# Optimization experiments

Measured on AMD Instinct MI355X. Metric: run time of the kernel, lower is better.

The kernel has to match this reference:

```python
import jax, jax.numpy as jnp
import numpy as np

LN_EPS = 1e-5

def setup_inputs() -> dict:
    key = jax.random.key(0)
    ks = jax.random.split(key, 4)
    B, D, H, K = 8192, 4096, 2048, 512
    return {
        "x": jax.random.normal(ks[0], (B, D), jnp.float32),
        "beta": jax.random.normal(ks[1], (D, K), jnp.float32) * 0.01,
        "compound_mean": jnp.zeros((D,), jnp.float32),
        "W1": jax.random.normal(ks[2], (H, D), jnp.float32) * 0.02,
        "b1": jnp.zeros((H,), jnp.float32),
        "ln_w": jnp.ones((H,), jnp.float32),
        "ln_b": jnp.zeros((H,), jnp.float32),
        "W2": jax.random.normal(ks[3], (K, H), jnp.float32) * 0.02,
        "b2": jnp.zeros((K,), jnp.float32),
    }

def reference(x, beta, compound_mean, W1, b1, ln_w, ln_b, W2, b2):
    # compound path of BiQBMVAE.forward (compound=True)
    h = jnp.einsum('bd,hd->bh', x - compound_mean, W1) + b1      # fc1
    mu = jnp.mean(h, axis=-1, keepdims=True)                      # LayerNorm
    var = jnp.mean(jnp.square(h - mu), axis=-1, keepdims=True)
    h = (h - mu) * jax.lax.rsqrt(var + LN_EPS) * ln_w + ln_b
    h = jax.nn.relu(h)                                            # act_fn
    q_logits = jnp.einsum('bh,kh->bk', h, W2) + b2                # fc2 -> [B, k]
    x_recon = jax.nn.sigmoid(jnp.einsum('bk,dk->bd', q_logits, beta))  # decode_compound
    return (q_logits, x_recon, q_logits, q_logits)
```

## Files before the change

kernel.cpp:

```cpp
#include <hip/hip_runtime.h>
#include <hip/hip_bf16.h>
#include <cstddef>
#include <cstdint>

#define LN_EPS 1e-5f

#define B_DIM 8192
#define D_DIM 4096
#define H_DIM 2048
#define K_DIM 512

typedef __bf16 bf16x8_t __attribute__((ext_vector_type(8)));
typedef float f32x4_t __attribute__((ext_vector_type(4)));

__device__ __forceinline__ void gl2lds16(const __hip_bfloat16* g,
                                         __hip_bfloat16* l) {
  __builtin_amdgcn_global_load_lds(
      (const __attribute__((address_space(1))) uint32_t*)g,
      (__attribute__((address_space(3))) uint32_t*)l, 16, 0, 0);
}

__global__ __launch_bounds__(256) void conv_x_kernel(
    const float* __restrict__ x, const float* __restrict__ cmean,
    __hip_bfloat16* __restrict__ out) {
  const long i = (((long)blockIdx.x << 8) + threadIdx.x) << 3;
  const int col = (int)(i & (D_DIM - 1));
  const float4 a = *(const float4*)(x + i);
  const float4 b = *(const float4*)(x + i + 4);
  const float4 ma = *(const float4*)(cmean + col);
  const float4 mb = *(const float4*)(cmean + col + 4);
  union { __hip_bfloat16 h[8]; uint4 u; } pk;
  pk.h[0] = __float2bfloat16(a.x - ma.x);
  pk.h[1] = __float2bfloat16(a.y - ma.y);
  pk.h[2] = __float2bfloat16(a.z - ma.z);
  pk.h[3] = __float2bfloat16(a.w - ma.w);
  pk.h[4] = __float2bfloat16(b.x - mb.x);
  pk.h[5] = __float2bfloat16(b.y - mb.y);
  pk.h[6] = __float2bfloat16(b.z - mb.z);
  pk.h[7] = __float2bfloat16(b.w - mb.w);
  *(uint4*)(out + i) = pk.u;
}

__global__ __launch_bounds__(256) void conv_w3_kernel(
    const float* __restrict__ W1, const float* __restrict__ W2,
    const float* __restrict__ beta, __hip_bfloat16* __restrict__ W1b,
    __hip_bfloat16* __restrict__ W2b, __hip_bfloat16* __restrict__ betab) {
  const int blk = blockIdx.x;
  const float* src;
  __hip_bfloat16* dst;
  long base;
  if (blk < 4096) {
    src = W1; dst = W1b; base = blk;
  } else if (blk < 4608) {
    src = W2; dst = W2b; base = blk - 4096;
  } else {
    src = beta; dst = betab; base = blk - 4608;
  }
  const long i = ((base << 8) + threadIdx.x) << 3;
  const float4 a = *(const float4*)(src + i);
  const float4 b = *(const float4*)(src + i + 4);
  union { __hip_bfloat16 h[8]; uint4 u; } pk;
  pk.h[0] = __float2bfloat16(a.x);
  pk.h[1] = __float2bfloat16(a.y);
  pk.h[2] = __float2bfloat16(a.z);
  pk.h[3] = __float2bfloat16(a.w);
  pk.h[4] = __float2bfloat16(b.x);
  pk.h[5] = __float2bfloat16(b.y);
  pk.h[6] = __float2bfloat16(b.z);
  pk.h[7] = __float2bfloat16(b.w);
  *(uint4*)(dst + i) = pk.u;
}

template <int EPI>
__global__ __launch_bounds__(256) void gemm_bt(
    const __hip_bfloat16* __restrict__ A, int lda,
    const __hip_bfloat16* __restrict__ Bm, int ldb,
    const float* __restrict__ bias, float* __restrict__ C0, int ldc,
    float* __restrict__ C2, float* __restrict__ C3,
    __hip_bfloat16* __restrict__ Cb, int Kd) {
  __shared__ __hip_bfloat16 lA[128 * 32];
  __shared__ __hip_bfloat16 lB[128 * 32];

  const int t = threadIdx.x;
  const int lane = t & 63;
  const int wv = t >> 6;
  const int wm = (wv >> 1) * 64;
  const int wn = (wv & 1) * 64;
  const int fr = lane & 15;
  const int ko = lane >> 4;
  const int kos = (ko ^ ((fr >> 1) & 3)) * 8;

  const long rowA = (long)blockIdx.y * 128;
  const long rowB = (long)blockIdx.x * 128;

  const int ci = wv * 128 + lane;
  const int srow = ci >> 2;
  const int scol = (((ci & 3) ^ ((ci >> 3) & 3))) * 8;
  const __hip_bfloat16* pA0 = A + (rowA + srow) * (long)lda + scol;
  const __hip_bfloat16* pA1 = pA0 + 16L * lda;
  const __hip_bfloat16* pB0 = Bm + (rowB + srow) * (long)ldb + scol;
  const __hip_bfloat16* pB1 = pB0 + 16L * ldb;
  __hip_bfloat16* lA0 = lA + wv * 128 * 8;
  __hip_bfloat16* lA1 = lA0 + 64 * 8;
  __hip_bfloat16* lB0 = lB + wv * 128 * 8;
  __hip_bfloat16* lB1 = lB0 + 64 * 8;

  f32x4_t acc[4][4];
  const f32x4_t zero = {0.f, 0.f, 0.f, 0.f};
#pragma unroll
  for (int mi = 0; mi < 4; ++mi)
#pragma unroll
    for (int ni = 0; ni < 4; ++ni) acc[mi][ni] = zero;

  for (int k0 = 0; k0 < Kd; k0 += 32) {
    gl2lds16(pA0 + k0, lA0);
    gl2lds16(pA1 + k0, lA1);
    gl2lds16(pB0 + k0, lB0);
    gl2lds16(pB1 + k0, lB1);
    __syncthreads();

    bf16x8_t af[4], bfv[4];
#pragma unroll
    for (int mi = 0; mi < 4; ++mi)
      af[mi] = *(const bf16x8_t*)&lA[(wm + mi * 16 + fr) * 32 + kos];
#pragma unroll
    for (int ni = 0; ni < 4; ++ni)
      bfv[ni] = *(const bf16x8_t*)&lB[(wn + ni * 16 + fr) * 32 + kos];
#pragma unroll
    for (int mi = 0; mi < 4; ++mi)
#pragma unroll
      for (int ni = 0; ni < 4; ++ni)
        acc[mi][ni] = __builtin_amdgcn_mfma_f32_16x16x32_bf16(
            af[mi], bfv[ni], acc[mi][ni], 0, 0, 0);
    __syncthreads();
  }

  const long cRow0 = rowA + wm;
  const int cCol0 = (int)rowB + wn;
#pragma unroll
  for (int mi = 0; mi < 4; ++mi) {
#pragma unroll
    for (int ni = 0; ni < 4; ++ni) {
      f32x4_t a = acc[mi][ni];
      int col = cCol0 + ni * 16 + fr;
#pragma unroll
      for (int r = 0; r < 4; ++r) {
        long row = cRow0 + mi * 16 + ko * 4 + r;
        float val = a[r];
        if constexpr (EPI == 0) {
          val += bias[col];
          C0[row * (long)ldc + col] = val;
        } else if constexpr (EPI == 1) {
          val += bias[col];
          C0[row * (long)ldc + col] = val;
          C2[row * (long)ldc + col] = val;
          C3[row * (long)ldc + col] = val;
          Cb[row * (long)ldc + col] = __float2bfloat16(val);
        } else {
          val = 1.f / (1.f + __expf(-val));
          C0[row * (long)ldc + col] = val;
        }
      }
    }
  }
}

__global__ __launch_bounds__(256) void ln_relu_kernel(
    void* hptr, const float* __restrict__ ln_w, const float* __restrict__ ln_b) {
  const int H = H_DIM;
  float* h = (float*)hptr;
  __hip_bfloat16* hb = (__hip_bfloat16*)hptr;

  const long row = blockIdx.x;
  const int t = threadIdx.x;
  const int lane = t & 63;
  const int wv = t >> 6;
  const float* hr = h + row * H;

  float v[8];
#pragma unroll
  for (int i = 0; i < 8; ++i) v[i] = hr[t + i * 256];

  __shared__ float red[8];

  float s = 0.f;
#pragma unroll
  for (int i = 0; i < 8; ++i) s += v[i];
#pragma unroll
  for (int off = 32; off; off >>= 1) s += __shfl_down(s, off);
  if (lane == 0) red[wv] = s;
  __syncthreads();
  const float mu = (red[0] + red[1] + red[2] + red[3]) * (1.f / (float)H);

  float vs = 0.f;
#pragma unroll
  for (int i = 0; i < 8; ++i) {
    float d = v[i] - mu;
    vs += d * d;
  }
#pragma unroll
  for (int off = 32; off; off >>= 1) vs += __shfl_down(vs, off);
  if (lane == 0) red[4 + wv] = vs;
  __syncthreads();
  const float var = (red[4] + red[5] + red[6] + red[7]) * (1.f / (float)H);
  const float rs = rsqrtf(var + LN_EPS);

  __hip_bfloat16* hbr = hb + row * (long)D_DIM;
#pragma unroll
  for (int i = 0; i < 8; ++i) {
    int col = t + i * 256;
    float y = (v[i] - mu) * rs * ln_w[col] + ln_b[col];
    y = fmaxf(y, 0.f);
    hbr[col] = __float2bfloat16(y);
  }
}

extern "C" void kernel_launch(void* const* d_in, const int* in_sizes, int n_in,
                              void* d_out, int out_size, void* d_ws,
                              size_t ws_size, hipStream_t stream) {
  const float* x = (const float*)d_in[0];
  const float* beta = (const float*)d_in[1];
  const float* cmean = (const float*)d_in[2];
  const float* W1 = (const float*)d_in[3];
  const float* b1 = (const float*)d_in[4];
  const float* ln_w = (const float*)d_in[5];
  const float* ln_b = (const float*)d_in[6];
  const float* W2 = (const float*)d_in[7];
  const float* b2 = (const float*)d_in[8];

  float* out = (float*)d_out;
  float* q0 = out;
  float* xr = out + (size_t)B_DIM * K_DIM;
  float* q2 = xr + (size_t)B_DIM * D_DIM;
  float* q3 = q2 + (size_t)B_DIM * K_DIM;

  __hip_bfloat16* xb = (__hip_bfloat16*)xr;
  float* h = xr + (size_t)B_DIM * D_DIM / 2;
  __hip_bfloat16* hb = (__hip_bfloat16*)h;

  __hip_bfloat16* W1b = (__hip_bfloat16*)d_ws;
  __hip_bfloat16* W2b = W1b + (size_t)H_DIM * D_DIM;
  __hip_bfloat16* betab = W2b + (size_t)K_DIM * H_DIM;
  __hip_bfloat16* qb = betab + (size_t)D_DIM * K_DIM;

  dim3 blk(256, 1, 1);

  hipLaunchKernelGGL(conv_x_kernel, dim3((B_DIM * (size_t)D_DIM) / 2048), blk,
                     0, stream, x, cmean, xb);
  hipLaunchKernelGGL(conv_w3_kernel, dim3(4096 + 512 + 1024), blk, 0, stream,
                     W1, W2, beta, W1b, W2b, betab);

  hipLaunchKernelGGL((gemm_bt<0>), dim3(H_DIM / 128, B_DIM / 128), blk, 0,
                     stream, xb, D_DIM, W1b, D_DIM, b1, h, H_DIM,
                     (float*)nullptr, (float*)nullptr,
                     (__hip_bfloat16*)nullptr, D_DIM);

  hipLaunchKernelGGL(ln_relu_kernel, dim3(B_DIM), blk, 0, stream, (void*)h,
                     ln_w, ln_b);

  hipLaunchKernelGGL((gemm_bt<1>), dim3(K_DIM / 128, B_DIM / 128), blk, 0,
                     stream, hb, D_DIM, W2b, H_DIM, b2, q0, K_DIM, q2, q3, qb,
                     H_DIM);

  hipLaunchKernelGGL((gemm_bt<2>), dim3(D_DIM / 128, B_DIM / 128), blk, 0,
                     stream, qb, K_DIM, betab, K_DIM, (const float*)nullptr,
                     xr, D_DIM, (float*)nullptr, (float*)nullptr,
                     (__hip_bfloat16*)nullptr, K_DIM);
}
```

Measured before the change: 638.0 us.

## Use 256x256 tile GEMM with triple-buffered LDS pipeline for fc1 and decode

Adds a new 512-thread GEMM kernel with 256x256 output tiles, a three-slot LDS ring buffer fed by direct global-to-LDS loads with a prefetch distance of two, an XOR-swizzled LDS layout, and setprio around the MFMA blocks. It replaces the 128x128 GEMM for the fc1 and sigmoid-decode stages. The goal is more data reuse per loaded tile and better overlap of loads with MFMA. In exchange it needs 128 accumulator registers per thread and 96KB of LDS, and the grid becomes smaller.

```diff
diff --git a/kernel.cpp b/kernel.cpp
--- a/kernel.cpp
+++ b/kernel.cpp
@@ -165,6 +165,146 @@
   }
 }
 
+template <int EPI>
+__global__ __launch_bounds__(512, 2) void gemm256_bt(
+    const __hip_bfloat16* __restrict__ A, int lda,
+    const __hip_bfloat16* __restrict__ Bm, int ldb,
+    const float* __restrict__ bias, float* __restrict__ C0, int ldc, int Kd) {
+  constexpr int SLOT = 16384;
+  __shared__ __hip_bfloat16 lds[3 * SLOT];
+
+  const int t_ = threadIdx.x;
+  const int lane = t_ & 63;
+  const int wv = t_ >> 6;
+  const int wr = wv >> 2;
+  const int wc = wv & 3;
+  const int fr = lane & 15;
+  const int ko = lane >> 4;
+  const int kos = (ko ^ ((fr >> 1) & 3)) * 8;
+
+  const long rowA = (long)blockIdx.y * 256;
+  const long rowB = (long)blockIdx.x * 256;
+
+  const int ci = (wv << 6) + lane;
+  const int srow = ci >> 2;
+  const int scol = ((ci & 3) ^ ((ci >> 3) & 3)) << 3;
+  const __hip_bfloat16* pA0 = A + (rowA + srow) * (long)lda + scol;
+  const __hip_bfloat16* pA1 = pA0 + 128L * lda;
+  const __hip_bfloat16* pB0 = Bm + (rowB + srow) * (long)ldb + scol;
+  const __hip_bfloat16* pB1 = pB0 + 128L * ldb;
+
+  f32x4_t acc[8][4];
+  const f32x4_t zero = {0.f, 0.f, 0.f, 0.f};
+#pragma unroll
+  for (int mi = 0; mi < 8; ++mi)
+#pragma unroll
+    for (int ni = 0; ni < 4; ++ni) acc[mi][ni] = zero;
+
+  const int NT = Kd >> 5;
+
+  {
+    __hip_bfloat16* a0 = lds + wv * 512;
+    gl2lds16(pA0, a0);
+    gl2lds16(pA1, a0 + 4096);
+    __hip_bfloat16* b0 = lds + 8192 + wv * 512;
+    gl2lds16(pB0, b0);
+    gl2lds16(pB1, b0 + 4096);
+  }
+  if (NT > 1) {
+    __hip_bfloat16* a1 = lds + SLOT + wv * 512;
+    gl2lds16(pA0 + 32, a1);
+    gl2lds16(pA1 + 32, a1 + 4096);
+    __hip_bfloat16* b1 = lds + SLOT + 8192 + wv * 512;
+    gl2lds16(pB0 + 32, b1);
+    gl2lds16(pB1 + 32, b1 + 4096);
+    asm volatile("s_waitcnt vmcnt(4)" ::: "memory");
+  } else {
+    asm volatile("s_waitcnt vmcnt(0)" ::: "memory");
+  }
+  __builtin_amdgcn_s_barrier();
+  __builtin_amdgcn_sched_barrier(0);
+
+  for (int t = 0; t < NT; ++t) {
+    const int slot = t % 3;
+    const int nslot = (t + 2) % 3;
+    const __hip_bfloat16* sA = lds + slot * SLOT;
+    const __hip_bfloat16* sB = sA + 8192;
+    const int kk = (t + 2) << 5;
+    const bool pf = (t + 2) < NT;
+
+    bf16x8_t af[4], bfv[4];
+#pragma unroll
+    for (int mi = 0; mi < 4; ++mi)
+      af[mi] = *(const bf16x8_t*)&sA[(wr * 128 + mi * 16 + fr) * 32 + kos];
+#pragma unroll
+    for (int ni = 0; ni < 4; ++ni)
+      bfv[ni] = *(const bf16x8_t*)&sB[(wc * 64 + ni * 16 + fr) * 32 + kos];
+    if (pf) {
+      __hip_bfloat16* la = lds + nslot * SLOT + wv * 512;
+      gl2lds16(pA0 + kk, la);
+      gl2lds16(pA1 + kk, la + 4096);
+    }
+    __builtin_amdgcn_s_setprio(1);
+#pragma unroll
+    for (int mi = 0; mi < 4; ++mi)
+#pragma unroll
+      for (int ni = 0; ni < 4; ++ni)
+        acc[mi][ni] = __builtin_amdgcn_mfma_f32_16x16x32_bf16(
+            af[mi], bfv[ni], acc[mi][ni], 0, 0, 0);
+    __builtin_amdgcn_s_setprio(0);
+
+    bf16x8_t ag[4];
+#pragma unroll
+    for (int mi = 0; mi < 4; ++mi)
+      ag[mi] =
+          *(const bf16x8_t*)&sA[(wr * 128 + 64 + mi * 16 + fr) * 32 + kos];
+    if (pf) {
+      __hip_bfloat16* lb = lds + nslot * SLOT + 8192 + wv * 512;
+      gl2lds16(pB0 + kk, lb);
+      gl2lds16(pB1 + kk, lb + 4096);
+    }
+    __builtin_amdgcn_s_setprio(1);
+#pragma unroll
+    for (int mi = 0; mi < 4; ++mi)
+#pragma unroll
+      for (int ni = 0; ni < 4; ++ni)
+        acc[4 + mi][ni] = __builtin_amdgcn_mfma_f32_16x16x32_bf16(
+            ag[mi], bfv[ni], acc[4 + mi][ni], 0, 0, 0);
+    __builtin_amdgcn_s_setprio(0);
+
+    if (t + 1 < NT) {
+      if (pf)
+        asm volatile("s_waitcnt vmcnt(4)" ::: "memory");
+      else
+        asm volatile("s_waitcnt vmcnt(0)" ::: "memory");
+      __builtin_amdgcn_s_barrier();
+      __builtin_amdgcn_sched_barrier(0);
+    }
+  }
+
+  const long cRow0 = rowA + wr * 128;
+  const int cCol0 = (int)rowB + wc * 64;
+#pragma unroll
+  for (int mi = 0; mi < 8; ++mi) {
+#pragma unroll
+    for (int ni = 0; ni < 4; ++ni) {
+      f32x4_t a = acc[mi][ni];
+      const int col = cCol0 + ni * 16 + fr;
+#pragma unroll
+      for (int r = 0; r < 4; ++r) {
+        const long row = cRow0 + mi * 16 + ko * 4 + r;
+        float val = a[r];
+        if constexpr (EPI == 0) {
+          val += bias[col];
+        } else {
+          val = 1.f / (1.f + __expf(-val));
+        }
+        C0[row * (long)ldc + col] = val;
+      }
+    }
+  }
+}
+
 __global__ __launch_bounds__(256) void ln_relu_kernel(
     void* hptr, const float* __restrict__ ln_w, const float* __restrict__ ln_b) {
   const int H = H_DIM;
@@ -244,16 +384,15 @@
   __hip_bfloat16* qb = betab + (size_t)D_DIM * K_DIM;
 
   dim3 blk(256, 1, 1);
+  dim3 blk512(512, 1, 1);
 
   hipLaunchKernelGGL(conv_x_kernel, dim3((B_DIM * (size_t)D_DIM) / 2048), blk,
                      0, stream, x, cmean, xb);
   hipLaunchKernelGGL(conv_w3_kernel, dim3(4096 + 512 + 1024), blk, 0, stream,
                      W1, W2, beta, W1b, W2b, betab);
 
-  hipLaunchKernelGGL((gemm_bt<0>), dim3(H_DIM / 128, B_DIM / 128), blk, 0,
-                     stream, xb, D_DIM, W1b, D_DIM, b1, h, H_DIM,
-                     (float*)nullptr, (float*)nullptr,
-                     (__hip_bfloat16*)nullptr, D_DIM);
+  hipLaunchKernelGGL((gemm256_bt<0>), dim3(H_DIM / 256, B_DIM / 256), blk512,
+                     0, stream, xb, D_DIM, W1b, D_DIM, b1, h, H_DIM, D_DIM);
 
   hipLaunchKernelGGL(ln_relu_kernel, dim3(B_DIM), blk, 0, stream, (void*)h,
                      ln_w, ln_b);
@@ -262,8 +401,7 @@
                      stream, hb, D_DIM, W2b, H_DIM, b2, q0, K_DIM, q2, q3, qb,
                      H_DIM);
 
-  hipLaunchKernelGGL((gemm_bt<2>), dim3(D_DIM / 128, B_DIM / 128), blk, 0,
-                     stream, qb, K_DIM, betab, K_DIM, (const float*)nullptr,
-                     xr, D_DIM, (float*)nullptr, (float*)nullptr,
-                     (__hip_bfloat16*)nullptr, K_DIM);
-}
+  hipLaunchKernelGGL((gemm256_bt<2>), dim3(D_DIM / 256, B_DIM / 256), blk512,
+                     0, stream, qb, K_DIM, betab, K_DIM, (const float*)nullptr,
+                     xr, D_DIM, K_DIM);
+}
```

Result: faster. 546.2 us (-14.4%).

## Add 256x256 eight-wave pipelined GEMM for fc1 and decode, remap block order

Applied to the files above, without the earlier changes.

Adds a new GEMM kernel with 256x256 tiles, 512 threads and double-buffered LDS (128 KB) fed by direct global-to-LDS loads. Its staged loads are interleaved with MFMA phases and use s_setprio to favour the matrix instructions. It replaces the 128x128 kernel for the two large GEMMs (fc1 and the sigmoid decode), aiming for higher arithmetic intensity and better latency hiding. It also remaps the workgroup index in both GEMM kernels (an XCD-style interleave) to improve L2 locality across chiplets. The cost is heavy register and LDS use, which limits occupancy, plus many barriers per iteration.

```diff
diff --git a/kernel.cpp b/kernel.cpp
--- a/kernel.cpp
+++ b/kernel.cpp
@@ -90,8 +90,15 @@
   const int ko = lane >> 4;
   const int kos = (ko ^ ((fr >> 1) & 3)) * 8;
 
-  const long rowA = (long)blockIdx.y * 128;
-  const long rowB = (long)blockIdx.x * 128;
+  const int gx = gridDim.x;
+  const int nwg = gx * gridDim.y;
+  const int f = blockIdx.y * gx + blockIdx.x;
+  const int w = (f & 7) * (nwg >> 3) + (f >> 3);
+  const int bx = w % gx;
+  const int by = w / gx;
+
+  const long rowA = (long)by * 128;
+  const long rowB = (long)bx * 128;
 
   const int ci = wv * 128 + lane;
   const int srow = ci >> 2;
@@ -165,6 +172,199 @@
   }
 }
 
+template <int EPI>
+__global__ __launch_bounds__(512, 2) void gemm256_8p(
+    const __hip_bfloat16* __restrict__ A, int lda,
+    const __hip_bfloat16* __restrict__ Bm, int ldb,
+    const float* __restrict__ bias, float* __restrict__ C0, int ldc, int Kd) {
+  __shared__ __hip_bfloat16 lds[65536];
+
+  const int t_ = threadIdx.x;
+  const int lane = t_ & 63;
+  const int wv = t_ >> 6;
+  const int wr = wv >> 2;
+  const int wc = wv & 3;
+  const int fr = lane & 15;
+  const int ko = lane >> 4;
+
+  const int gx = gridDim.x;
+  const int nwg = gx * gridDim.y;
+  const int f = blockIdx.y * gx + blockIdx.x;
+  const int w = (f & 7) * (nwg >> 3) + (f >> 3);
+  const int bx = w % gx;
+  const int by = w / gx;
+
+  const long rowA = (long)by * 256;
+  const long rowB = (long)bx * 256;
+
+  const int p1 = (wv << 6) + lane;
+  const int row1 = p1 >> 3;
+  const int kq1 = (p1 & 7) ^ ((p1 >> 4) & 7);
+  const __hip_bfloat16* sA0 = A + (rowA + row1) * (long)lda + kq1 * 8;
+  const __hip_bfloat16* sA1 = A + (rowA + 128 + row1) * (long)lda + kq1 * 8;
+  const __hip_bfloat16* sB0 = Bm + (rowB + row1) * (long)ldb + kq1 * 8;
+  const __hip_bfloat16* sB1 = Bm + (rowB + 128 + row1) * (long)ldb + kq1 * 8;
+  const long stepA = 64L * lda;
+  const long stepB = 64L * ldb;
+
+  auto STG = [&](const __hip_bfloat16* src, long step, int slotElem, int kofs) {
+    __hip_bfloat16* d = lds + slotElem + wv * 512;
+    gl2lds16(src + kofs, d);
+    gl2lds16(src + step + kofs, d + 4096);
+  };
+
+  const int aSlotOff = wr * 8192;
+  const int bSlotOff = 16384 + (wc >> 1) * 8192;
+  const int lcB = (wc & 1) * 64;
+  const int ck0 = (ko ^ (fr >> 1)) * 8;
+  const int ck1 = ((4 + ko) ^ (fr >> 1)) * 8;
+
+  auto LDA4 = [&](bf16x8_t(&dst)[4][2], int base, int rbase) {
+#pragma unroll
+    for (int mi = 0; mi < 4; ++mi) {
+      const int ro = base + (rbase + mi * 16 + fr) * 64;
+      dst[mi][0] = *(const bf16x8_t*)&lds[ro + ck0];
+      dst[mi][1] = *(const bf16x8_t*)&lds[ro + ck1];
+    }
+  };
+  auto LDB2 = [&](bf16x8_t(&dst)[2][2], int base, int cbase) {
+#pragma unroll
+    for (int ni = 0; ni < 2; ++ni) {
+      const int co = base + (cbase + ni * 16 + fr) * 64;
+      dst[ni][0] = *(const bf16x8_t*)&lds[co + ck0];
+      dst[ni][1] = *(const bf16x8_t*)&lds[co + ck1];
+    }
+  };
+
+  f32x4_t acc[8][4];
+  const f32x4_t zero = {0.f, 0.f, 0.f, 0.f};
+#pragma unroll
+  for (int a = 0; a < 8; ++a)
+#pragma unroll
+    for (int b = 0; b < 4; ++b) acc[a][b] = zero;
+
+  auto MMA16 = [&](int amh, int anh, bf16x8_t(&aa)[4][2], bf16x8_t(&bb)[2][2]) {
+    __builtin_amdgcn_s_setprio(1);
+#pragma unroll
+    for (int mi = 0; mi < 4; ++mi)
+#pragma unroll
+      for (int ni = 0; ni < 2; ++ni)
+#pragma unroll
+        for (int kh = 0; kh < 2; ++kh)
+          acc[amh * 4 + mi][anh * 2 + ni] =
+              __builtin_amdgcn_mfma_f32_16x16x32_bf16(
+                  aa[mi][kh], bb[ni][kh], acc[amh * 4 + mi][anh * 2 + ni], 0,
+                  0, 0);
+    __builtin_amdgcn_s_setprio(0);
+  };
+
+#define BAR __builtin_amdgcn_s_barrier()
+#define LGKM0                                          \
+  {                                                    \
+    asm volatile("s_waitcnt lgkmcnt(0)" ::: "memory"); \
+    __builtin_amdgcn_sched_barrier(0);                 \
+  }
+
+  STG(sA0, stepA, 0, 0);
+  STG(sA1, stepA, 8192, 0);
+  STG(sB0, stepB, 16384, 0);
+  STG(sB1, stepB, 24576, 0);
+  STG(sB0, stepB, 32768 + 16384, 64);
+  STG(sB1, stepB, 32768 + 24576, 64);
+  asm volatile("s_waitcnt vmcnt(4)" ::: "memory");
+  BAR;
+
+  bf16x8_t af[4][2], ag[4][2], b0[2][2], b1[2][2];
+  const int NI = Kd >> 7;
+  for (int i = 0; i < NI; ++i) {
+    const int k0 = i << 7;
+    const bool pf = (i + 1) < NI;
+
+    LDA4(af, aSlotOff, 0);
+    LDB2(b0, bSlotOff, lcB);
+    STG(sA0, stepA, 32768, k0 + 64);
+    BAR;
+    LGKM0;
+    MMA16(0, 0, af, b0);
+    BAR;
+
+    LDB2(b1, bSlotOff, lcB + 32);
+    STG(sA1, stepA, 32768 + 8192, k0 + 64);
+    BAR;
+    LGKM0;
+    MMA16(0, 1, af, b1);
+    BAR;
+
+    LDA4(ag, aSlotOff, 64);
+    if (pf) STG(sB0, stepB, 16384, k0 + 128);
+    BAR;
+    LGKM0;
+    MMA16(1, 0, ag, b0);
+    BAR;
+
+    if (pf) STG(sB1, stepB, 24576, k0 + 128);
+    BAR;
+    MMA16(1, 1, ag, b1);
+    if (pf)
+      asm volatile("s_waitcnt vmcnt(4)" ::: "memory");
+    else
+      asm volatile("s_waitcnt vmcnt(0)" ::: "memory");
+    BAR;
+
+    LDA4(af, 32768 + aSlotOff, 0);
+    LDB2(b0, 32768 + bSlotOff, lcB);
+    if (pf) STG(sA0, stepA, 0, k0 + 128);
+    BAR;
+    LGKM0;
+    MMA16(0, 0, af, b0);
+    BAR;
+
+    LDB2(b1, 32768 + bSlotOff, lcB + 32);
+    if (pf) STG(sA1, stepA, 8192, k0 + 128);
+    BAR;
+    LGKM0;
+    MMA16(0, 1, af, b1);
+    BAR;
+
+    LDA4(ag, 32768 + aSlotOff, 64);
+    if (pf) STG(sB0, stepB, 32768 + 16384, k0 + 192);
+    BAR;
+    LGKM0;
+    MMA16(1, 0, ag, b0);
+    BAR;
+
+    if (pf) STG(sB1, stepB, 32768 + 24576, k0 + 192);
+    BAR;
+    MMA16(1, 1, ag, b1);
+    if (pf) asm volatile("s_waitcnt vmcnt(4)" ::: "memory");
+    BAR;
+  }
+#undef BAR
+#undef LGKM0
+
+  const long cRow0 = rowA + wr * 128;
+  const int cCol0 = (int)rowB + wc * 64;
+#pragma unroll
+  for (int a = 0; a < 8; ++a) {
+#pragma unroll
+    for (int b = 0; b < 4; ++b) {
+      f32x4_t v4 = acc[a][b];
+      const int col = cCol0 + b * 16 + fr;
+#pragma unroll
+      for (int r = 0; r < 4; ++r) {
+        const long row = cRow0 + a * 16 + ko * 4 + r;
+        float val = v4[r];
+        if constexpr (EPI == 0) {
+          val += bias[col];
+        } else {
+          val = 1.f / (1.f + __expf(-val));
+        }
+        C0[row * (long)ldc + col] = val;
+      }
+    }
+  }
+}
+
 __global__ __launch_bounds__(256) void ln_relu_kernel(
     void* hptr, const float* __restrict__ ln_w, const float* __restrict__ ln_b) {
   const int H = H_DIM;
@@ -244,16 +444,15 @@
   __hip_bfloat16* qb = betab + (size_t)D_DIM * K_DIM;
 
   dim3 blk(256, 1, 1);
+  dim3 blk512(512, 1, 1);
 
   hipLaunchKernelGGL(conv_x_kernel, dim3((B_DIM * (size_t)D_DIM) / 2048), blk,
                      0, stream, x, cmean, xb);
   hipLaunchKernelGGL(conv_w3_kernel, dim3(4096 + 512 + 1024), blk, 0, stream,
                      W1, W2, beta, W1b, W2b, betab);
 
-  hipLaunchKernelGGL((gemm_bt<0>), dim3(H_DIM / 128, B_DIM / 128), blk, 0,
-                     stream, xb, D_DIM, W1b, D_DIM, b1, h, H_DIM,
-                     (float*)nullptr, (float*)nullptr,
-                     (__hip_bfloat16*)nullptr, D_DIM);
+  hipLaunchKernelGGL((gemm256_8p<0>), dim3(H_DIM / 256, B_DIM / 256), blk512,
+                     0, stream, xb, D_DIM, W1b, D_DIM, b1, h, H_DIM, D_DIM);
 
   hipLaunchKernelGGL(ln_relu_kernel, dim3(B_DIM), blk, 0, stream, (void*)h,
                      ln_w, ln_b);
@@ -262,8 +461,7 @@
                      stream, hb, D_DIM, W2b, H_DIM, b2, q0, K_DIM, q2, q3, qb,
                      H_DIM);
 
-  hipLaunchKernelGGL((gemm_bt<2>), dim3(D_DIM / 128, B_DIM / 128), blk, 0,
-                     stream, qb, K_DIM, betab, K_DIM, (const float*)nullptr,
-                     xr, D_DIM, (float*)nullptr, (float*)nullptr,
-                     (__hip_bfloat16*)nullptr, K_DIM);
-}
+  hipLaunchKernelGGL((gemm256_8p<2>), dim3(D_DIM / 256, B_DIM / 256), blk512,
+                     0, stream, qb, K_DIM, betab, K_DIM, (const float*)nullptr,
+                     xr, D_DIM, K_DIM);
+}
```

Result: faster. 532.0 us (-16.6%).
